# Kernel optimization log

Hardware: AMD Instinct MI355X
Metric: run time of the kernel (lower is better)

The kernel has to match this reference:

```python
import jax, jax.numpy as jnp
import numpy as np
from jax import lax

B, N, C = 8, 4096, 64
RATIO = 0.25
M = int(N * RATIO)          # sampled centers per cloud (fps ratio)
K = 64                      # max_num_neighbors in ball query
R = 0.2                     # ball_query_radius
H = 128                     # MLP width
NEG = jnp.float32(-1e30)


def setup_inputs() -> dict:
    key = jax.random.key(0)
    k1, k2, k3, k4 = jax.random.split(key, 4)
    x = jax.random.normal(k1, (B, N, C), jnp.float32)
    pos = jax.random.uniform(k2, (B, N, 3), jnp.float32)  # unit cube coords
    W1 = jax.random.normal(k3, (C + 3, H), jnp.float32) * 0.05
    b1 = jnp.zeros((H,), jnp.float32)
    W2 = jax.random.normal(k4, (H, H), jnp.float32) * 0.05
    b2 = jnp.zeros((H,), jnp.float32)
    return {"x": x, "pos": pos, "W1": W1, "b1": b1, "W2": W2, "b2": b2}


def _fps(pos):
    """Farthest point sampling on one cloud [N,3] -> M int32 indices (start at 0)."""
    d0 = jnp.sum((pos - pos[0]) ** 2, axis=-1)  # min sq-dist to selected set
    def step(mind, _):
        nxt = jnp.argmax(mind).astype(jnp.int32)
        d = jnp.sum((pos - pos[nxt]) ** 2, axis=-1)
        return jnp.minimum(mind, d), nxt
    _, idxs = lax.scan(step, d0, None, length=M - 1)
    return jnp.concatenate([jnp.zeros((1,), jnp.int32), idxs])


def reference(x, pos, W1, b1, W2, b2):
    # --- FPS sampling (per cloud, deterministic start) ---
    idx = jax.vmap(_fps)(pos)                      # [B,M]
    bidx = jnp.arange(B)[:, None]
    centers = pos[bidx, idx]                        # [B,M,3]

    # --- ball query: first K points within radius R of each center ---
    d2 = jnp.sum((centers[:, :, None, :] - pos[:, None, :, :]) ** 2, axis=-1)  # [B,M,N]
    in_ball = d2 <= R * R
    # prefer lowest index (torch_cluster radius returns up to K arbitrary/first hits)
    score = jnp.where(in_ball, -jnp.arange(N, dtype=jnp.float32), NEG)
    vals, nbr = lax.top_k(score, K)                 # nbr: [B,M,K] neighbor indices
    valid = vals > NEG / 2                          # [B,M,K]; center itself always valid

    # --- PointNetConv: gather -> local MLP on [x_j, pos_j - pos_i] -> max aggr ---
    b3 = jnp.arange(B)[:, None, None]
    xj = x[b3, nbr]                                  # [B,M,K,C]
    rel = pos[b3, nbr] - centers[:, :, None, :]      # [B,M,K,3]
    feat = jnp.concatenate([xj, rel], axis=-1)       # [B,M,K,C+3]
    h = jax.nn.relu(feat @ W1 + b1)
    h = jax.nn.relu(h @ W2 + b2)                     # [B,M,K,H]
    h = jnp.where(valid[..., None], h, NEG)
    out = jnp.max(h, axis=2)                          # [B,M,H] max aggregation
    return out, centers
```

## Files before the change

### kernel.cpp

```cpp
#include <hip/hip_runtime.h>

#define BN 8
#define NN 4096
#define CC 64
#define MM 1024
#define KK 64
#define HH 128

typedef __attribute__((ext_vector_type(8))) short short8;
typedef __attribute__((ext_vector_type(4))) float f32x4;
typedef __attribute__((ext_vector_type(2))) float f32x2;
typedef unsigned long long u64;
typedef unsigned int u32;

__device__ inline unsigned short f2bf(float f) {
  union { float f; unsigned u; } v; v.f = f;
  unsigned r = v.u + 0x7FFFu + ((v.u >> 16) & 1u);
  return (unsigned short)(r >> 16);
}

__device__ inline float sqd(float ax, float ay, float az, float bx, float by, float bz) {
  float dx = __fsub_rn(ax, bx), dy = __fsub_rn(ay, by), dz = __fsub_rn(az, bz);
  return __fadd_rn(__fadd_rn(__fmul_rn(dx, dx), __fmul_rn(dy, dy)), __fmul_rn(dz, dz));
}

__global__ void prep_w(const float* __restrict__ W1, const float* __restrict__ W2,
                       short* __restrict__ W1T, short* __restrict__ W2T) {
  int t = blockIdx.x * 256 + threadIdx.x;
  if (t < 128 * 104) {
    int n = t / 104, k = t % 104;
    float v = (k < 67) ? W1[k * 128 + n] : 0.f;
    W1T[t] = (short)f2bf(v);
  }
  if (t < 128 * 136) {
    int n = t / 136, k = t % 136;
    float v = (k < 128) ? W2[k * 128 + n] : 0.f;
    W2T[t] = (short)f2bf(v);
  }
}

template <int CTRL, int RM>
__device__ __forceinline__ float dppf(float x) {
  int v = __builtin_amdgcn_update_dpp(0, __float_as_int(x), CTRL, RM, 0xF, false);
  return __int_as_float(v);
}

__device__ __forceinline__ float wave_fmax(float x) {
  x = fmaxf(x, dppf<0xB1, 0xF>(x));
  x = fmaxf(x, dppf<0x4E, 0xF>(x));
  x = fmaxf(x, dppf<0x141, 0xF>(x));
  x = fmaxf(x, dppf<0x140, 0xF>(x));
  x = fmaxf(x, dppf<0x142, 0xA>(x));
  x = fmaxf(x, dppf<0x143, 0xC>(x));
  return __int_as_float(__builtin_amdgcn_readlane(__float_as_int(x), 63));
}

__global__ __launch_bounds__(512) void fps_k(const float* __restrict__ pos,
                                             float* __restrict__ centers) {
  const int b = blockIdx.x;
  const int tid = threadIdx.x;
  const int lane = tid & 63;
  const int wv = tid >> 6;
  __shared__ f32x4 sp4[NN];
  __shared__ f32x4 svm4[2];
  __shared__ u32 sminp[2];

  const float* P = pos + (size_t)b * NN * 3;

  f32x2 X[4], Y[4], Z[4], M[4];
#pragma unroll
  for (int j = 0; j < 4; ++j) {
    int p0 = tid * 8 + j * 2;
    float x0 = P[p0 * 3 + 0], y0 = P[p0 * 3 + 1], z0 = P[p0 * 3 + 2];
    float x1 = P[p0 * 3 + 3], y1 = P[p0 * 3 + 4], z1 = P[p0 * 3 + 5];
    X[j].x = x0; X[j].y = x1;
    Y[j].x = y0; Y[j].y = y1;
    Z[j].x = z0; Z[j].y = z1;
    f32x4 v0; v0[0] = x0; v0[1] = y0; v0[2] = z0; v0[3] = 0.f;
    f32x4 v1; v1[0] = x1; v1[1] = y1; v1[2] = z1; v1[3] = 0.f;
    sp4[p0] = v0;
    sp4[p0 + 1] = v1;
  }
#pragma unroll
  for (int j = 0; j < 4; ++j)
    asm volatile("" : "+v"(X[j]), "+v"(Y[j]), "+v"(Z[j]));

  const float c0x = P[0], c0y = P[1], c0z = P[2];
  {
#pragma clang fp contract(off)
    f32x2 cx; cx.x = c0x; cx.y = c0x;
    f32x2 cy; cy.x = c0y; cy.y = c0y;
    f32x2 cz; cz.x = c0z; cz.y = c0z;
#pragma unroll
    for (int j = 0; j < 4; ++j) {
      f32x2 dx = X[j] - cx, dy = Y[j] - cy, dz = Z[j] - cz;
      M[j] = (dx * dx + dy * dy) + dz * dz;
    }
  }

  if (tid == 0) {
    centers[(size_t)(b * MM) * 3 + 0] = c0x;
    centers[(size_t)(b * MM) * 3 + 1] = c0y;
    centers[(size_t)(b * MM) * 3 + 2] = c0z;
    sminp[0] = 0xFFFFFFFFu;
    sminp[1] = 0xFFFFFFFFu;
  }
  __syncthreads();

  for (int m = 1; m < MM; ++m) {
    float mv = fmaxf(fmaxf(fmaxf(M[0].x, M[0].y), fmaxf(M[1].x, M[1].y)),
                     fmaxf(fmaxf(M[2].x, M[2].y), fmaxf(M[3].x, M[3].y)));
    float wmax = wave_fmax(mv);
    if (lane == 0) ((float*)svm4)[wv] = wmax;
    __syncthreads();
    f32x4 s0 = svm4[0], s1 = svm4[1];
    float bmax = fmaxf(fmaxf(fmaxf(s0[0], s0[1]), fmaxf(s0[2], s0[3])),
                       fmaxf(fmaxf(s1[0], s1[1]), fmaxf(s1[2], s1[3])));
    if (mv == bmax) {
      u32 em = 0;
#pragma unroll
      for (int j = 0; j < 4; ++j) {
        if (M[j].x == bmax) em |= 1u << (2 * j);
        if (M[j].y == bmax) em |= 1u << (2 * j + 1);
      }
      atomicMin(&sminp[m & 1], (u32)(tid * 8 + (int)__builtin_ctz(em)));
    }
    if (tid == 0) sminp[(m + 1) & 1] = 0xFFFFFFFFu;
    __syncthreads();
    const u32 bp = sminp[m & 1];
    const f32x4 c4 = sp4[bp];
    if (tid == 0) {
      centers[(size_t)(b * MM + m) * 3 + 0] = c4[0];
      centers[(size_t)(b * MM + m) * 3 + 1] = c4[1];
      centers[(size_t)(b * MM + m) * 3 + 2] = c4[2];
    }
    {
#pragma clang fp contract(off)
      f32x2 cx; cx.x = c4[0]; cx.y = c4[0];
      f32x2 cy; cy.x = c4[1]; cy.y = c4[1];
      f32x2 cz; cz.x = c4[2]; cz.y = c4[2];
#pragma unroll
      for (int j = 0; j < 4; ++j) {
        f32x2 dx = X[j] - cx, dy = Y[j] - cy, dz = Z[j] - cz;
        f32x2 d2 = (dx * dx + dy * dy) + dz * dz;
        M[j].x = fminf(M[j].x, d2.x);
        M[j].y = fminf(M[j].y, d2.y);
      }
    }
  }
}

__global__ __launch_bounds__(256) void sa_k(const float* __restrict__ x,
                                            const float* __restrict__ pos,
                                            const float* __restrict__ b1,
                                            const float* __restrict__ b2,
                                            const short* __restrict__ W1T,
                                            const short* __restrict__ W2T,
                                            const float* __restrict__ centers,
                                            float* __restrict__ out) {
  const int cm = blockIdx.x;
  const int b = cm >> 10;
  const int tid = threadIdx.x;
  const int lane = tid & 63, wv = tid >> 6;
  const int l15 = lane & 15, lg = lane >> 4;

  __shared__ short s_feat[64][104];
  __shared__ short s_h1[64][136];
  __shared__ int s_nbr[64];
  __shared__ int s_wcnt[4];

  const int n0 = wv * 32;
  short8 w1f[2][3], w2f[2][4];
#pragma unroll
  for (int nt = 0; nt < 2; ++nt) {
    int row = n0 + nt * 16 + l15;
#pragma unroll
    for (int kt = 0; kt < 3; ++kt)
      w1f[nt][kt] = *reinterpret_cast<const short8*>(W1T + row * 104 + kt * 32 + lg * 8);
#pragma unroll
    for (int kt = 0; kt < 4; ++kt)
      w2f[nt][kt] = *reinterpret_cast<const short8*>(W2T + row * 136 + kt * 32 + lg * 8);
  }

  const float* Pb = pos + (size_t)b * NN * 3;
  const float cx = centers[(size_t)cm * 3 + 0];
  const float cy = centers[(size_t)cm * 3 + 1];
  const float cz = centers[(size_t)cm * 3 + 2];

  int cnt = 0;
  for (int base = 0; base < NN; base += 256) {
    int p = base + tid;
    float d2 = sqd(Pb[p * 3 + 0], Pb[p * 3 + 1], Pb[p * 3 + 2], cx, cy, cz);
    bool pred = d2 <= 0.04f;
    unsigned long long mask = __ballot(pred);
    if (lane == 0) s_wcnt[wv] = __popcll(mask);
    __syncthreads();
    int wbase = cnt, tot = 0;
#pragma unroll
    for (int w = 0; w < 4; ++w) {
      int c = s_wcnt[w];
      tot += c;
      if (w < wv) wbase += c;
    }
    if (pred) {
      int slot = wbase + (int)__popcll(mask & ((1ull << lane) - 1ull));
      if (slot < KK) s_nbr[slot] = p;
    }
    cnt += tot;
    __syncthreads();
    if (cnt >= KK) break;
  }
  if (cnt > KK) cnt = KK;

  {
    int* fz = (int*)&s_feat[0][0];
    for (int i = tid; i < 64 * 104 / 2; i += 256) fz[i] = 0;
  }
  __syncthreads();

  {
    const int j = tid >> 2, q = tid & 3;
    if (j < cnt) {
      int nj = s_nbr[j];
      const float* xr = x + ((size_t)b * NN + nj) * CC + q * 16;
      unsigned* dst = (unsigned*)&s_feat[j][q * 16];
#pragma unroll
      for (int v4 = 0; v4 < 4; ++v4) {
        f32x4 xv = *reinterpret_cast<const f32x4*>(xr + v4 * 4);
        unsigned lo0 = (unsigned)f2bf(xv[0]) | ((unsigned)f2bf(xv[1]) << 16);
        unsigned lo1 = (unsigned)f2bf(xv[2]) | ((unsigned)f2bf(xv[3]) << 16);
        dst[v4 * 2 + 0] = lo0;
        dst[v4 * 2 + 1] = lo1;
      }
      if (q == 0) {
        s_feat[j][64] = (short)f2bf(__fsub_rn(Pb[nj * 3 + 0], cx));
        s_feat[j][65] = (short)f2bf(__fsub_rn(Pb[nj * 3 + 1], cy));
        s_feat[j][66] = (short)f2bf(__fsub_rn(Pb[nj * 3 + 2], cz));
      }
    }
  }
  __syncthreads();

  f32x4 acc[4][2];
#pragma unroll
  for (int mt = 0; mt < 4; ++mt)
#pragma unroll
    for (int nt = 0; nt < 2; ++nt) acc[mt][nt] = (f32x4)0.f;

#pragma unroll
  for (int mt = 0; mt < 4; ++mt) {
    int arow = mt * 16 + l15;
#pragma unroll
    for (int kt = 0; kt < 3; ++kt) {
      short8 af = *reinterpret_cast<const short8*>(&s_feat[arow][kt * 32 + lg * 8]);
      acc[mt][0] = __builtin_amdgcn_mfma_f32_16x16x32_bf16(af, w1f[0][kt], acc[mt][0], 0, 0, 0);
      acc[mt][1] = __builtin_amdgcn_mfma_f32_16x16x32_bf16(af, w1f[1][kt], acc[mt][1], 0, 0, 0);
    }
  }

#pragma unroll
  for (int mt = 0; mt < 4; ++mt) {
#pragma unroll
    for (int nt = 0; nt < 2; ++nt) {
      int col = n0 + nt * 16 + l15;
      float bias = b1[col];
#pragma unroll
      for (int r = 0; r < 4; ++r) {
        int row = mt * 16 + lg * 4 + r;
        float h = fmaxf(__fadd_rn(acc[mt][nt][r], bias), 0.f);
        s_h1[row][col] = (short)f2bf(h);
      }
    }
  }
  __syncthreads();

  f32x4 acc2[4][2];
#pragma unroll
  for (int mt = 0; mt < 4; ++mt)
#pragma unroll
    for (int nt = 0; nt < 2; ++nt) acc2[mt][nt] = (f32x4)0.f;

#pragma unroll
  for (int mt = 0; mt < 4; ++mt) {
    int arow = mt * 16 + l15;
#pragma unroll
    for (int kt = 0; kt < 4; ++kt) {
      short8 af = *reinterpret_cast<const short8*>(&s_h1[arow][kt * 32 + lg * 8]);
      acc2[mt][0] = __builtin_amdgcn_mfma_f32_16x16x32_bf16(af, w2f[0][kt], acc2[mt][0], 0, 0, 0);
      acc2[mt][1] = __builtin_amdgcn_mfma_f32_16x16x32_bf16(af, w2f[1][kt], acc2[mt][1], 0, 0, 0);
    }
  }

#pragma unroll
  for (int nt = 0; nt < 2; ++nt) {
    int col = n0 + nt * 16 + l15;
    float bias = b2[col];
    float mx = -1e30f;
#pragma unroll
    for (int mt = 0; mt < 4; ++mt) {
#pragma unroll
      for (int r = 0; r < 4; ++r) {
        int row = mt * 16 + lg * 4 + r;
        float h = fmaxf(__fadd_rn(acc2[mt][nt][r], bias), 0.f);
        if (row < cnt) mx = fmaxf(mx, h);
      }
    }
    mx = fmaxf(mx, __shfl_xor(mx, 16));
    mx = fmaxf(mx, __shfl_xor(mx, 32));
    if (lg == 0) out[(size_t)cm * HH + col] = mx;
  }
}

extern "C" void kernel_launch(void* const* d_in, const int* in_sizes, int n_in,
                              void* d_out, int out_size, void* d_ws, size_t ws_size,
                              hipStream_t stream) {
  const float* x = (const float*)d_in[0];
  const float* pos = (const float*)d_in[1];
  const float* W1 = (const float*)d_in[2];
  const float* b1 = (const float*)d_in[3];
  const float* W2 = (const float*)d_in[4];
  const float* b2 = (const float*)d_in[5];

  float* out = (float*)d_out;
  float* centers = out + (size_t)BN * MM * HH;

  char* ws = (char*)d_ws;
  short* W1T = (short*)ws;
  short* W2T = (short*)(ws + 26624);

  prep_w<<<68, 256, 0, stream>>>(W1, W2, W1T, W2T);
  fps_k<<<BN, 512, 0, stream>>>(pos, centers);
  sa_k<<<BN * MM, 256, 0, stream>>>(x, pos, b1, b2, W1T, W2T, centers, out);
}
```

Baseline: 834.1 us.

## Use packed value-index keys in FPS to drop atomic and second barrier

```diff
diff --git a/kernel.cpp b/kernel.cpp
--- a/kernel.cpp
+++ b/kernel.cpp
@@ -12,6 +12,7 @@
 typedef __attribute__((ext_vector_type(2))) float f32x2;
 typedef unsigned long long u64;
 typedef unsigned int u32;
+typedef __attribute__((ext_vector_type(2))) u64 u64x2;
 
 __device__ inline unsigned short f2bf(float f) {
   union { float f; unsigned u; } v; v.f = f;
@@ -55,15 +56,17 @@
   return __int_as_float(__builtin_amdgcn_readlane(__float_as_int(x), 63));
 }
 
+__device__ __forceinline__ u64 kmax(u64 a, u64 b) { return a > b ? a : b; }
+
 __global__ __launch_bounds__(512) void fps_k(const float* __restrict__ pos,
                                              float* __restrict__ centers) {
   const int b = blockIdx.x;
   const int tid = threadIdx.x;
   const int lane = tid & 63;
   const int wv = tid >> 6;
-  __shared__ f32x4 sp4[NN];
-  __shared__ f32x4 svm4[2];
-  __shared__ u32 sminp[2];
+  __shared__ float spx[NN], spy[NN], spz[NN];
+  __shared__ __align__(16) u64 svk[2][8];
+  __shared__ u32 sidx[MM];
 
   const float* P = pos + (size_t)b * NN * 3;
 
@@ -76,10 +79,9 @@
     X[j].x = x0; X[j].y = x1;
     Y[j].x = y0; Y[j].y = y1;
     Z[j].x = z0; Z[j].y = z1;
-    f32x4 v0; v0[0] = x0; v0[1] = y0; v0[2] = z0; v0[3] = 0.f;
-    f32x4 v1; v1[0] = x1; v1[1] = y1; v1[2] = z1; v1[3] = 0.f;
-    sp4[p0] = v0;
-    sp4[p0 + 1] = v1;
+    spx[p0] = x0; spx[p0 + 1] = x1;
+    spy[p0] = y0; spy[p0 + 1] = y1;
+    spz[p0] = z0; spz[p0 + 1] = z1;
   }
 #pragma unroll
   for (int j = 0; j < 4; ++j)
@@ -97,48 +99,41 @@
       M[j] = (dx * dx + dy * dy) + dz * dz;
     }
   }
-
-  if (tid == 0) {
-    centers[(size_t)(b * MM) * 3 + 0] = c0x;
-    centers[(size_t)(b * MM) * 3 + 1] = c0y;
-    centers[(size_t)(b * MM) * 3 + 2] = c0z;
-    sminp[0] = 0xFFFFFFFFu;
-    sminp[1] = 0xFFFFFFFFu;
-  }
+  if (tid == 0) sidx[0] = 0;
   __syncthreads();
 
   for (int m = 1; m < MM; ++m) {
-    float mv = fmaxf(fmaxf(fmaxf(M[0].x, M[0].y), fmaxf(M[1].x, M[1].y)),
-                     fmaxf(fmaxf(M[2].x, M[2].y), fmaxf(M[3].x, M[3].y)));
+    f32x2 mm = __builtin_elementwise_max(__builtin_elementwise_max(M[0], M[1]),
+                                         __builtin_elementwise_max(M[2], M[3]));
+    float mv = fmaxf(mm.x, mm.y);
     float wmax = wave_fmax(mv);
-    if (lane == 0) ((float*)svm4)[wv] = wmax;
+    u64 bal = __ballot(mv == wmax);
+    int L = (int)__builtin_ctzll(bal);
+    u32 em = 0;
+#pragma unroll
+    for (int j = 0; j < 4; ++j) {
+      if (M[j].x == mv) em |= 1u << (2 * j);
+      if (M[j].y == mv) em |= 1u << (2 * j + 1);
+    }
+    u32 lidx = (u32)(tid * 8) + (u32)__builtin_ctz(em);
+    u32 widx = (u32)__builtin_amdgcn_readlane((int)lidx, L);
+    if (lane == 0)
+      svk[m & 1][wv] = ((u64)__float_as_uint(wmax) << 32) | (u64)(u32)~widx;
     __syncthreads();
-    f32x4 s0 = svm4[0], s1 = svm4[1];
-    float bmax = fmaxf(fmaxf(fmaxf(s0[0], s0[1]), fmaxf(s0[2], s0[3])),
-                       fmaxf(fmaxf(s1[0], s1[1]), fmaxf(s1[2], s1[3])));
-    if (mv == bmax) {
-      u32 em = 0;
-#pragma unroll
-      for (int j = 0; j < 4; ++j) {
-        if (M[j].x == bmax) em |= 1u << (2 * j);
-        if (M[j].y == bmax) em |= 1u << (2 * j + 1);
-      }
-      atomicMin(&sminp[m & 1], (u32)(tid * 8 + (int)__builtin_ctz(em)));
-    }
-    if (tid == 0) sminp[(m + 1) & 1] = 0xFFFFFFFFu;
-    __syncthreads();
-    const u32 bp = sminp[m & 1];
-    const f32x4 c4 = sp4[bp];
-    if (tid == 0) {
-      centers[(size_t)(b * MM + m) * 3 + 0] = c4[0];
-      centers[(size_t)(b * MM + m) * 3 + 1] = c4[1];
-      centers[(size_t)(b * MM + m) * 3 + 2] = c4[2];
-    }
+    const u64x2 a0 = *(const u64x2*)&svk[m & 1][0];
+    const u64x2 a1 = *(const u64x2*)&svk[m & 1][2];
+    const u64x2 a2 = *(const u64x2*)&svk[m & 1][4];
+    const u64x2 a3 = *(const u64x2*)&svk[m & 1][6];
+    u64 kb = kmax(kmax(kmax(a0.x, a0.y), kmax(a1.x, a1.y)),
+                  kmax(kmax(a2.x, a2.y), kmax(a3.x, a3.y)));
+    const u32 bp = ~(u32)kb;
+    if (tid == 0) sidx[m] = bp;
+    const float ncx = spx[bp], ncy = spy[bp], ncz = spz[bp];
     {
 #pragma clang fp contract(off)
-      f32x2 cx; cx.x = c4[0]; cx.y = c4[0];
-      f32x2 cy; cy.x = c4[1]; cy.y = c4[1];
-      f32x2 cz; cz.x = c4[2]; cz.y = c4[2];
+      f32x2 cx; cx.x = ncx; cx.y = ncx;
+      f32x2 cy; cy.x = ncy; cy.y = ncy;
+      f32x2 cz; cz.x = ncz; cz.y = ncz;
 #pragma unroll
       for (int j = 0; j < 4; ++j) {
         f32x2 dx = X[j] - cx, dy = Y[j] - cy, dz = Z[j] - cz;
@@ -147,6 +142,14 @@
         M[j].y = fminf(M[j].y, d2.y);
       }
     }
+  }
+  __syncthreads();
+  for (int m = tid; m < MM; m += 512) {
+    u32 p = sidx[m];
+    size_t o = (size_t)(b * MM + m) * 3;
+    centers[o + 0] = spx[p];
+    centers[o + 1] = spy[p];
+    centers[o + 2] = spz[p];
   }
 }
 
```

Result: faster. 757.4 us (-9.2%).

## Restructure FPS: two clouds per block, one barrier per step via packed argmax keys

Applied to the files above, without the earlier changes.

```diff
diff --git a/kernel.cpp b/kernel.cpp
--- a/kernel.cpp
+++ b/kernel.cpp
@@ -55,98 +55,152 @@
   return __int_as_float(__builtin_amdgcn_readlane(__float_as_int(x), 63));
 }
 
-__global__ __launch_bounds__(512) void fps_k(const float* __restrict__ pos,
-                                             float* __restrict__ centers) {
-  const int b = blockIdx.x;
+__device__ __forceinline__ double keyd(f32x4 e) {
+  f32x2 p; p.x = e[0]; p.y = e[1];
+  return __builtin_bit_cast(double, p);
+}
+
+__device__ __forceinline__ void reduce_phase(float mv, const f32x2 (&X)[8], const f32x2 (&Y)[8],
+                                             const f32x2 (&Z)[8], const f32x2 (&M)[8],
+                                             int tid, int lane, int wv,
+                                             f32x4* svec_slot, float* svz_slot) {
+  float wmax = wave_fmax(mv);
+  u64 bal = __ballot(mv == wmax);
+  int L = (int)__builtin_ctzll(bal);
+  u32 em = 0;
+#pragma unroll
+  for (int j = 0; j < 8; ++j) {
+    if (M[j].x == mv) em |= 1u << (2 * j);
+    if (M[j].y == mv) em |= 1u << (2 * j + 1);
+  }
+  u32 eo = (u32)__builtin_ctz(em);
+  u32 jj = eo >> 1;
+  f32x2 xs = jj == 0 ? X[0] : jj == 1 ? X[1] : jj == 2 ? X[2] : jj == 3 ? X[3]
+           : jj == 4 ? X[4] : jj == 5 ? X[5] : jj == 6 ? X[6] : X[7];
+  f32x2 ys = jj == 0 ? Y[0] : jj == 1 ? Y[1] : jj == 2 ? Y[2] : jj == 3 ? Y[3]
+           : jj == 4 ? Y[4] : jj == 5 ? Y[5] : jj == 6 ? Y[6] : Y[7];
+  f32x2 zs = jj == 0 ? Z[0] : jj == 1 ? Z[1] : jj == 2 ? Z[2] : jj == 3 ? Z[3]
+           : jj == 4 ? Z[4] : jj == 5 ? Z[5] : jj == 6 ? Z[6] : Z[7];
+  float lx = (eo & 1) ? xs.y : xs.x;
+  float ly = (eo & 1) ? ys.y : ys.x;
+  float lz = (eo & 1) ? zs.y : zs.x;
+  if (lane == L) {
+    f32x4 ev;
+    ev[0] = __uint_as_float(~(u32)(tid * 16 + eo));
+    ev[1] = wmax;
+    ev[2] = lx;
+    ev[3] = ly;
+    svec_slot[wv] = ev;
+    svz_slot[wv] = lz;
+  }
+}
+
+__device__ __forceinline__ float resolve_update(f32x2 (&X)[8], f32x2 (&Y)[8], f32x2 (&Z)[8],
+                                                f32x2 (&M)[8], const f32x4* svec_slot,
+                                                const float* svz_slot, int tid, int m,
+                                                float* scen_b) {
+  f32x4 e0 = svec_slot[0], e1 = svec_slot[1], e2 = svec_slot[2], e3 = svec_slot[3];
+  f32x4 zv = *(const f32x4*)svz_slot;
+  double kb = fmax(fmax(keyd(e0), keyd(e1)), fmax(keyd(e2), keyd(e3)));
+  u64 kbu = __builtin_bit_cast(u64, kb);
+  u32 bp = ~(u32)kbu;
+  u32 w = bp >> 10;
+  float s0 = (w & 1) ? e1[2] : e0[2], s1 = (w & 1) ? e3[2] : e2[2];
+  float ncx = (w & 2) ? s1 : s0;
+  float t0 = (w & 1) ? e1[3] : e0[3], t1 = (w & 1) ? e3[3] : e2[3];
+  float ncy = (w & 2) ? t1 : t0;
+  float u0 = (w & 1) ? zv[1] : zv[0], u1 = (w & 1) ? zv[3] : zv[2];
+  float ncz = (w & 2) ? u1 : u0;
+  if (tid == 0) {
+    scen_b[m * 3 + 0] = ncx;
+    scen_b[m * 3 + 1] = ncy;
+    scen_b[m * 3 + 2] = ncz;
+  }
+  f32x2 rm;
+  {
+#pragma clang fp contract(off)
+    f32x2 vcx; vcx.x = ncx; vcx.y = ncx;
+    f32x2 vcy; vcy.x = ncy; vcy.y = ncy;
+    f32x2 vcz; vcz.x = ncz; vcz.y = ncz;
+#pragma unroll
+    for (int j = 0; j < 8; ++j) {
+      f32x2 dx = X[j] - vcx, dy = Y[j] - vcy, dz = Z[j] - vcz;
+      f32x2 d2 = (dx * dx + dy * dy) + dz * dz;
+      M[j] = __builtin_elementwise_min(M[j], d2);
+      rm = j ? __builtin_elementwise_max(rm, M[j]) : M[j];
+    }
+  }
+  return fmaxf(rm.x, rm.y);
+}
+
+__device__ __forceinline__ float init_m(const f32x2 (&X)[8], const f32x2 (&Y)[8],
+                                        const f32x2 (&Z)[8], f32x2 (&M)[8],
+                                        float cx, float cy, float cz) {
+  f32x2 rm;
+  {
+#pragma clang fp contract(off)
+    f32x2 vcx; vcx.x = cx; vcx.y = cx;
+    f32x2 vcy; vcy.x = cy; vcy.y = cy;
+    f32x2 vcz; vcz.x = cz; vcz.y = cz;
+#pragma unroll
+    for (int j = 0; j < 8; ++j) {
+      f32x2 dx = X[j] - vcx, dy = Y[j] - vcy, dz = Z[j] - vcz;
+      M[j] = (dx * dx + dy * dy) + dz * dz;
+      rm = j ? __builtin_elementwise_max(rm, M[j]) : M[j];
+    }
+  }
+  return fmaxf(rm.x, rm.y);
+}
+
+__global__ __launch_bounds__(256) void fps2_k(const float* __restrict__ pos,
+                                              float* __restrict__ centers) {
+  const int bA = blockIdx.x * 2, bB = bA + 1;
   const int tid = threadIdx.x;
   const int lane = tid & 63;
   const int wv = tid >> 6;
-  __shared__ f32x4 sp4[NN];
-  __shared__ f32x4 svm4[2];
-  __shared__ u32 sminp[2];
-
-  const float* P = pos + (size_t)b * NN * 3;
-
-  f32x2 X[4], Y[4], Z[4], M[4];
-#pragma unroll
-  for (int j = 0; j < 4; ++j) {
-    int p0 = tid * 8 + j * 2;
-    float x0 = P[p0 * 3 + 0], y0 = P[p0 * 3 + 1], z0 = P[p0 * 3 + 2];
-    float x1 = P[p0 * 3 + 3], y1 = P[p0 * 3 + 4], z1 = P[p0 * 3 + 5];
-    X[j].x = x0; X[j].y = x1;
-    Y[j].x = y0; Y[j].y = y1;
-    Z[j].x = z0; Z[j].y = z1;
-    f32x4 v0; v0[0] = x0; v0[1] = y0; v0[2] = z0; v0[3] = 0.f;
-    f32x4 v1; v1[0] = x1; v1[1] = y1; v1[2] = z1; v1[3] = 0.f;
-    sp4[p0] = v0;
-    sp4[p0 + 1] = v1;
-  }
-#pragma unroll
-  for (int j = 0; j < 4; ++j)
-    asm volatile("" : "+v"(X[j]), "+v"(Y[j]), "+v"(Z[j]));
-
-  const float c0x = P[0], c0y = P[1], c0z = P[2];
-  {
-#pragma clang fp contract(off)
-    f32x2 cx; cx.x = c0x; cx.y = c0x;
-    f32x2 cy; cy.x = c0y; cy.y = c0y;
-    f32x2 cz; cz.x = c0z; cz.y = c0z;
-#pragma unroll
-    for (int j = 0; j < 4; ++j) {
-      f32x2 dx = X[j] - cx, dy = Y[j] - cy, dz = Z[j] - cz;
-      M[j] = (dx * dx + dy * dy) + dz * dz;
-    }
-  }
-
+  __shared__ __align__(16) f32x4 svec[2][2][4];
+  __shared__ __align__(16) float svz[2][2][4];
+  __shared__ float scen[2][MM * 3];
+
+  const float* PA = pos + (size_t)bA * NN * 3;
+  const float* PB = pos + (size_t)bB * NN * 3;
+
+  f32x2 XA[8], YA[8], ZA[8], MA[8], XB[8], YB[8], ZB[8], MB[8];
+#pragma unroll
+  for (int j = 0; j < 8; ++j) {
+    int p0 = tid * 16 + j * 2;
+    XA[j].x = PA[p0 * 3 + 0]; YA[j].x = PA[p0 * 3 + 1]; ZA[j].x = PA[p0 * 3 + 2];
+    XA[j].y = PA[p0 * 3 + 3]; YA[j].y = PA[p0 * 3 + 4]; ZA[j].y = PA[p0 * 3 + 5];
+    XB[j].x = PB[p0 * 3 + 0]; YB[j].x = PB[p0 * 3 + 1]; ZB[j].x = PB[p0 * 3 + 2];
+    XB[j].y = PB[p0 * 3 + 3]; YB[j].y = PB[p0 * 3 + 4]; ZB[j].y = PB[p0 * 3 + 5];
+  }
+#pragma unroll
+  for (int j = 0; j < 8; ++j) {
+    asm volatile("" : "+v"(XA[j]), "+v"(YA[j]), "+v"(ZA[j]));
+    asm volatile("" : "+v"(XB[j]), "+v"(YB[j]), "+v"(ZB[j]));
+  }
+
+  const float cAx = PA[0], cAy = PA[1], cAz = PA[2];
+  const float cBx = PB[0], cBy = PB[1], cBz = PB[2];
+  float mvA = init_m(XA, YA, ZA, MA, cAx, cAy, cAz);
+  float mvB = init_m(XB, YB, ZB, MB, cBx, cBy, cBz);
   if (tid == 0) {
-    centers[(size_t)(b * MM) * 3 + 0] = c0x;
-    centers[(size_t)(b * MM) * 3 + 1] = c0y;
-    centers[(size_t)(b * MM) * 3 + 2] = c0z;
-    sminp[0] = 0xFFFFFFFFu;
-    sminp[1] = 0xFFFFFFFFu;
+    scen[0][0] = cAx; scen[0][1] = cAy; scen[0][2] = cAz;
+    scen[1][0] = cBx; scen[1][1] = cBy; scen[1][2] = cBz;
+  }
+
+  for (int m = 1; m < MM; ++m) {
+    const int pp = m & 1;
+    reduce_phase(mvA, XA, YA, ZA, MA, tid, lane, wv, &svec[pp][0][0], &svz[pp][0][0]);
+    reduce_phase(mvB, XB, YB, ZB, MB, tid, lane, wv, &svec[pp][1][0], &svz[pp][1][0]);
+    __syncthreads();
+    mvA = resolve_update(XA, YA, ZA, MA, &svec[pp][0][0], &svz[pp][0][0], tid, m, scen[0]);
+    mvB = resolve_update(XB, YB, ZB, MB, &svec[pp][1][0], &svz[pp][1][0], tid, m, scen[1]);
   }
   __syncthreads();
-
-  for (int m = 1; m < MM; ++m) {
-    float mv = fmaxf(fmaxf(fmaxf(M[0].x, M[0].y), fmaxf(M[1].x, M[1].y)),
-                     fmaxf(fmaxf(M[2].x, M[2].y), fmaxf(M[3].x, M[3].y)));
-    float wmax = wave_fmax(mv);
-    if (lane == 0) ((float*)svm4)[wv] = wmax;
-    __syncthreads();
-    f32x4 s0 = svm4[0], s1 = svm4[1];
-    float bmax = fmaxf(fmaxf(fmaxf(s0[0], s0[1]), fmaxf(s0[2], s0[3])),
-                       fmaxf(fmaxf(s1[0], s1[1]), fmaxf(s1[2], s1[3])));
-    if (mv == bmax) {
-      u32 em = 0;
-#pragma unroll
-      for (int j = 0; j < 4; ++j) {
-        if (M[j].x == bmax) em |= 1u << (2 * j);
-        if (M[j].y == bmax) em |= 1u << (2 * j + 1);
-      }
-      atomicMin(&sminp[m & 1], (u32)(tid * 8 + (int)__builtin_ctz(em)));
-    }
-    if (tid == 0) sminp[(m + 1) & 1] = 0xFFFFFFFFu;
-    __syncthreads();
-    const u32 bp = sminp[m & 1];
-    const f32x4 c4 = sp4[bp];
-    if (tid == 0) {
-      centers[(size_t)(b * MM + m) * 3 + 0] = c4[0];
-      centers[(size_t)(b * MM + m) * 3 + 1] = c4[1];
-      centers[(size_t)(b * MM + m) * 3 + 2] = c4[2];
-    }
-    {
-#pragma clang fp contract(off)
-      f32x2 cx; cx.x = c4[0]; cx.y = c4[0];
-      f32x2 cy; cy.x = c4[1]; cy.y = c4[1];
-      f32x2 cz; cz.x = c4[2]; cz.y = c4[2];
-#pragma unroll
-      for (int j = 0; j < 4; ++j) {
-        f32x2 dx = X[j] - cx, dy = Y[j] - cy, dz = Z[j] - cz;
-        f32x2 d2 = (dx * dx + dy * dy) + dz * dz;
-        M[j].x = fminf(M[j].x, d2.x);
-        M[j].y = fminf(M[j].y, d2.y);
-      }
-    }
+  for (int i = tid; i < MM * 3; i += 256) {
+    centers[(size_t)bA * MM * 3 + i] = scen[0][i];
+    centers[(size_t)bB * MM * 3 + i] = scen[1][i];
   }
 }
 
@@ -329,6 +383,6 @@
   short* W2T = (short*)(ws + 26624);
 
   prep_w<<<68, 256, 0, stream>>>(W1, W2, W1T, W2T);
-  fps_k<<<BN, 512, 0, stream>>>(pos, centers);
+  fps2_k<<<BN / 2, 256, 0, stream>>>(pos, centers);
   sa_k<<<BN * MM, 256, 0, stream>>>(x, pos, b1, b2, W1T, W2T, centers, out);
 }
```

Result: slower. 3.011 ms (+261.0%).

## Use single-barrier FPS argmax with packed 64-bit keys and buffered center output

Applied to the files above, without the earlier changes.

```diff
diff --git a/kernel.cpp b/kernel.cpp
--- a/kernel.cpp
+++ b/kernel.cpp
@@ -55,15 +55,20 @@
   return __int_as_float(__builtin_amdgcn_readlane(__float_as_int(x), 63));
 }
 
+__device__ __forceinline__ double keyd(f32x4 e) {
+  f32x2 p; p.x = e[0]; p.y = e[1];
+  return __builtin_bit_cast(double, p);
+}
+
 __global__ __launch_bounds__(512) void fps_k(const float* __restrict__ pos,
                                              float* __restrict__ centers) {
   const int b = blockIdx.x;
   const int tid = threadIdx.x;
   const int lane = tid & 63;
   const int wv = tid >> 6;
-  __shared__ f32x4 sp4[NN];
-  __shared__ f32x4 svm4[2];
-  __shared__ u32 sminp[2];
+  __shared__ __align__(16) double svk[2][8];
+  __shared__ __align__(16) f32x4 svc[2][8];
+  __shared__ float scen[MM * 3];
 
   const float* P = pos + (size_t)b * NN * 3;
 
@@ -71,83 +76,103 @@
 #pragma unroll
   for (int j = 0; j < 4; ++j) {
     int p0 = tid * 8 + j * 2;
-    float x0 = P[p0 * 3 + 0], y0 = P[p0 * 3 + 1], z0 = P[p0 * 3 + 2];
-    float x1 = P[p0 * 3 + 3], y1 = P[p0 * 3 + 4], z1 = P[p0 * 3 + 5];
-    X[j].x = x0; X[j].y = x1;
-    Y[j].x = y0; Y[j].y = y1;
-    Z[j].x = z0; Z[j].y = z1;
-    f32x4 v0; v0[0] = x0; v0[1] = y0; v0[2] = z0; v0[3] = 0.f;
-    f32x4 v1; v1[0] = x1; v1[1] = y1; v1[2] = z1; v1[3] = 0.f;
-    sp4[p0] = v0;
-    sp4[p0 + 1] = v1;
+    X[j].x = P[p0 * 3 + 0]; Y[j].x = P[p0 * 3 + 1]; Z[j].x = P[p0 * 3 + 2];
+    X[j].y = P[p0 * 3 + 3]; Y[j].y = P[p0 * 3 + 4]; Z[j].y = P[p0 * 3 + 5];
   }
 #pragma unroll
   for (int j = 0; j < 4; ++j)
     asm volatile("" : "+v"(X[j]), "+v"(Y[j]), "+v"(Z[j]));
 
   const float c0x = P[0], c0y = P[1], c0z = P[2];
+  float mv;
   {
 #pragma clang fp contract(off)
-    f32x2 cx; cx.x = c0x; cx.y = c0x;
-    f32x2 cy; cy.x = c0y; cy.y = c0y;
-    f32x2 cz; cz.x = c0z; cz.y = c0z;
+    f32x2 vcx; vcx.x = c0x; vcx.y = c0x;
+    f32x2 vcy; vcy.x = c0y; vcy.y = c0y;
+    f32x2 vcz; vcz.x = c0z; vcz.y = c0z;
+    f32x2 rm;
 #pragma unroll
     for (int j = 0; j < 4; ++j) {
-      f32x2 dx = X[j] - cx, dy = Y[j] - cy, dz = Z[j] - cz;
+      f32x2 dx = X[j] - vcx, dy = Y[j] - vcy, dz = Z[j] - vcz;
       M[j] = (dx * dx + dy * dy) + dz * dz;
-    }
-  }
-
-  if (tid == 0) {
-    centers[(size_t)(b * MM) * 3 + 0] = c0x;
-    centers[(size_t)(b * MM) * 3 + 1] = c0y;
-    centers[(size_t)(b * MM) * 3 + 2] = c0z;
-    sminp[0] = 0xFFFFFFFFu;
-    sminp[1] = 0xFFFFFFFFu;
-  }
+      rm = j ? __builtin_elementwise_max(rm, M[j]) : M[j];
+    }
+    mv = fmaxf(rm.x, rm.y);
+  }
+  if (tid == 0) { scen[0] = c0x; scen[1] = c0y; scen[2] = c0z; }
   __syncthreads();
 
   for (int m = 1; m < MM; ++m) {
-    float mv = fmaxf(fmaxf(fmaxf(M[0].x, M[0].y), fmaxf(M[1].x, M[1].y)),
-                     fmaxf(fmaxf(M[2].x, M[2].y), fmaxf(M[3].x, M[3].y)));
+    const int pp = m & 1;
     float wmax = wave_fmax(mv);
-    if (lane == 0) ((float*)svm4)[wv] = wmax;
+    u64 bal = __ballot(mv == wmax);
+    int L = (int)__builtin_ctzll(bal);
+    u32 em = 0;
+#pragma unroll
+    for (int j = 0; j < 4; ++j) {
+      if (M[j].x == mv) em |= 1u << (2 * j);
+      if (M[j].y == mv) em |= 1u << (2 * j + 1);
+    }
+    u32 eo = (u32)__builtin_ctz(em);
+    u32 jj = eo >> 1;
+    f32x2 xs = (jj & 2) ? ((jj & 1) ? X[3] : X[2]) : ((jj & 1) ? X[1] : X[0]);
+    f32x2 ys = (jj & 2) ? ((jj & 1) ? Y[3] : Y[2]) : ((jj & 1) ? Y[1] : Y[0]);
+    f32x2 zs = (jj & 2) ? ((jj & 1) ? Z[3] : Z[2]) : ((jj & 1) ? Z[1] : Z[0]);
+    float lx = (eo & 1) ? xs.y : xs.x;
+    float ly = (eo & 1) ? ys.y : ys.x;
+    float lz = (eo & 1) ? zs.y : zs.x;
+    if (lane == L) {
+      u64 kk = ((u64)__float_as_uint(wmax) << 32) | (u64)(u32)~(u32)(tid * 8 + eo);
+      svk[pp][wv] = __builtin_bit_cast(double, kk);
+      f32x4 cv; cv[0] = lx; cv[1] = ly; cv[2] = lz; cv[3] = 0.f;
+      svc[pp][wv] = cv;
+    }
     __syncthreads();
-    f32x4 s0 = svm4[0], s1 = svm4[1];
-    float bmax = fmaxf(fmaxf(fmaxf(s0[0], s0[1]), fmaxf(s0[2], s0[3])),
-                       fmaxf(fmaxf(s1[0], s1[1]), fmaxf(s1[2], s1[3])));
-    if (mv == bmax) {
-      u32 em = 0;
-#pragma unroll
-      for (int j = 0; j < 4; ++j) {
-        if (M[j].x == bmax) em |= 1u << (2 * j);
-        if (M[j].y == bmax) em |= 1u << (2 * j + 1);
-      }
-      atomicMin(&sminp[m & 1], (u32)(tid * 8 + (int)__builtin_ctz(em)));
-    }
-    if (tid == 0) sminp[(m + 1) & 1] = 0xFFFFFFFFu;
-    __syncthreads();
-    const u32 bp = sminp[m & 1];
-    const f32x4 c4 = sp4[bp];
+    const f32x4* kp = (const f32x4*)&svk[pp][0];
+    f32x4 k01 = kp[0], k23 = kp[1], k45 = kp[2], k67 = kp[3];
+    f32x4 q0 = svc[pp][0], q1 = svc[pp][1], q2 = svc[pp][2], q3 = svc[pp][3];
+    f32x4 q4 = svc[pp][4], q5 = svc[pp][5], q6 = svc[pp][6], q7 = svc[pp][7];
+    f32x2 klo, khi;
+    klo.x = k01[0]; klo.y = k01[1]; khi.x = k01[2]; khi.y = k01[3];
+    double d0 = __builtin_bit_cast(double, klo), d1 = __builtin_bit_cast(double, khi);
+    klo.x = k23[0]; klo.y = k23[1]; khi.x = k23[2]; khi.y = k23[3];
+    double d2 = __builtin_bit_cast(double, klo), d3 = __builtin_bit_cast(double, khi);
+    klo.x = k45[0]; klo.y = k45[1]; khi.x = k45[2]; khi.y = k45[3];
+    double d4 = __builtin_bit_cast(double, klo), d5 = __builtin_bit_cast(double, khi);
+    klo.x = k67[0]; klo.y = k67[1]; khi.x = k67[2]; khi.y = k67[3];
+    double d6 = __builtin_bit_cast(double, klo), d7 = __builtin_bit_cast(double, khi);
+    double kb = fmax(fmax(fmax(d0, d1), fmax(d2, d3)), fmax(fmax(d4, d5), fmax(d6, d7)));
+    u64 kbu = __builtin_bit_cast(u64, kb);
+    u32 w = (~(u32)kbu) >> 9;
+    f32x4 s0 = (w & 1) ? q1 : q0, s1 = (w & 1) ? q3 : q2;
+    f32x4 s2 = (w & 1) ? q5 : q4, s3 = (w & 1) ? q7 : q6;
+    f32x4 t0 = (w & 2) ? s1 : s0, t1 = (w & 2) ? s3 : s2;
+    f32x4 cw = (w & 4) ? t1 : t0;
+    const float ncx = cw[0], ncy = cw[1], ncz = cw[2];
     if (tid == 0) {
-      centers[(size_t)(b * MM + m) * 3 + 0] = c4[0];
-      centers[(size_t)(b * MM + m) * 3 + 1] = c4[1];
-      centers[(size_t)(b * MM + m) * 3 + 2] = c4[2];
+      scen[m * 3 + 0] = ncx;
+      scen[m * 3 + 1] = ncy;
+      scen[m * 3 + 2] = ncz;
     }
     {
 #pragma clang fp contract(off)
-      f32x2 cx; cx.x = c4[0]; cx.y = c4[0];
-      f32x2 cy; cy.x = c4[1]; cy.y = c4[1];
-      f32x2 cz; cz.x = c4[2]; cz.y = c4[2];
+      f32x2 vcx; vcx.x = ncx; vcx.y = ncx;
+      f32x2 vcy; vcy.x = ncy; vcy.y = ncy;
+      f32x2 vcz; vcz.x = ncz; vcz.y = ncz;
+      f32x2 rm;
 #pragma unroll
       for (int j = 0; j < 4; ++j) {
-        f32x2 dx = X[j] - cx, dy = Y[j] - cy, dz = Z[j] - cz;
+        f32x2 dx = X[j] - vcx, dy = Y[j] - vcy, dz = Z[j] - vcz;
         f32x2 d2 = (dx * dx + dy * dy) + dz * dz;
-        M[j].x = fminf(M[j].x, d2.x);
-        M[j].y = fminf(M[j].y, d2.y);
-      }
-    }
-  }
+        M[j] = __builtin_elementwise_min(M[j], d2);
+        rm = j ? __builtin_elementwise_max(rm, M[j]) : M[j];
+      }
+      mv = fmaxf(rm.x, rm.y);
+    }
+  }
+  __syncthreads();
+  for (int i = tid; i < MM * 3; i += 512)
+    centers[(size_t)b * MM * 3 + i] = scen[i];
 }
 
 __global__ __launch_bounds__(256) void sa_k(const float* __restrict__ x,
```

After: 1.138 ms. +36.4%, slower.
